# Kernel tuning notes

Measured on AMD Instinct MI355X. Metric: run time of the kernel, lower is better.

## Reference

```python
import jax, jax.numpy as jnp
import numpy as np
from jax import lax

B, C_IN, T = 256, 1, 1632
HID, CB_DIM, NUM_TOK, NUM_Q = 64, 512, 1024, 2


def conv_k2s2(x, W, b):
    # Conv1d(kernel=2, stride=2): x [B,Ci,T] -> [B,Co,T//2]; W [Co,Ci,2]
    Bx, Ci, Tx = x.shape
    xr = x.reshape(Bx, Ci, Tx // 2, 2)
    return jnp.einsum('bitk,oik->bot', xr, W) + b[None, :, None]


def convT_k2s2(x, W, b):
    # ConvTranspose1d(kernel=2, stride=2): x [B,Ci,T] -> [B,Co,2T]; W [Ci,Co,2] (torch layout)
    Bx, Ci, Tx = x.shape
    y = jnp.einsum('bit,iok->botk', x, W)  # [B,Co,T,2]
    Co = W.shape[1]
    return y.reshape(Bx, Co, 2 * Tx) + b[None, :, None]


def conv1x1(x, W, b):
    # W [Co,Ci]
    return jnp.einsum('bit,oi->bot', x, W) + b[None, :, None]


def residual_vq(x, codebooks):
    # x [B,t,D]; codebooks [NUM_Q, NUM_TOK, D]. Euclidean argmin + straight-through.
    residual = x
    quantized_out = jnp.zeros_like(x)
    all_idx, all_loss = [], []
    for q in range(codebooks.shape[0]):
        cb = codebooks[q]  # [N,D]
        # squared euclidean distance, single large GEMM
        d2 = (jnp.sum(residual ** 2, -1, keepdims=True)
              - 2.0 * jnp.einsum('btd,nd->btn', residual, cb)
              + jnp.sum(cb ** 2, -1))  # [B,t,N]
        idx = jnp.argmin(d2, axis=-1)  # [B,t]
        quant = cb[idx]  # gather [B,t,D]
        # commitment loss (codebook treated as fixed / EMA-updated)
        loss = jnp.mean((lax.stop_gradient(quant) - residual) ** 2)
        # straight-through estimator
        quant_st = residual + lax.stop_gradient(quant - residual)
        residual = residual - lax.stop_gradient(quant)
        quantized_out = quantized_out + quant_st
        all_idx.append(idx)
        all_loss.append(loss)
    return quantized_out, jnp.stack(all_idx, -1), jnp.stack(all_loss)


def setup_inputs() -> dict:
    key = jax.random.key(0)
    ks = jax.random.split(key, 16)
    s = 0.02
    return {
        'img': jax.random.normal(ks[0], (B, C_IN, T), jnp.float32),
        'W_e1': jax.random.normal(ks[1], (HID, C_IN, 2), jnp.float32) * s,
        'b_e1': jnp.zeros((HID,), jnp.float32),
        'W_e2': jax.random.normal(ks[2], (HID, HID, 2), jnp.float32) * s,
        'b_e2': jnp.zeros((HID,), jnp.float32),
        'W_e3': jax.random.normal(ks[3], (CB_DIM, HID), jnp.float32) * s,
        'b_e3': jnp.zeros((CB_DIM,), jnp.float32),
        'codebooks': jax.random.normal(ks[4], (NUM_Q, NUM_TOK, CB_DIM), jnp.float32),
        'Wt_d1': jax.random.normal(ks[5], (CB_DIM, HID, 2), jnp.float32) * s,
        'b_d1': jnp.zeros((HID,), jnp.float32),
        'Wt_d2': jax.random.normal(ks[6], (HID, HID, 2), jnp.float32) * s,
        'b_d2': jnp.zeros((HID,), jnp.float32),
        'W_d3': jax.random.normal(ks[7], (C_IN, HID), jnp.float32) * s,
        'b_d3': jnp.zeros((C_IN,), jnp.float32),
    }


def reference(img, W_e1, b_e1, W_e2, b_e2, W_e3, b_e3, codebooks,
              Wt_d1, b_d1, Wt_d2, b_d2, W_d3, b_d3):
    # encoder
    h = jax.nn.relu(conv_k2s2(img, W_e1, b_e1))
    h = jax.nn.relu(conv_k2s2(h, W_e2, b_e2))
    encoded = conv1x1(h, W_e3, b_e3)  # [B,512,408]
    # residual VQ over tokens
    x = jnp.transpose(encoded, (0, 2, 1))  # b c t -> b t c
    quantized, indices, commit_loss = residual_vq(x, codebooks)
    quantized = jnp.transpose(quantized, (0, 2, 1))  # b t c -> b c t
    # decoder
    d = jax.nn.relu(convT_k2s2(quantized, Wt_d1, b_d1))
    d = jax.nn.relu(convT_k2s2(d, Wt_d2, b_d2))
    out = conv1x1(d, W_d3, b_d3)  # [B,1,1632]
    recon_loss = jnp.mean((img - out) ** 2)
    return out, recon_loss, commit_loss, indices, quantized
```

## Files before the change

### kernel.cpp

```cpp
#include <hip/hip_runtime.h>

#define NB    256
#define TLEN  1632
#define HIDC  64
#define CBD   512
#define NTOK  1024
#define T2L   816
#define T4L   408
#define MTOK  (NB*T4L)
#define M2TOK (NB*T2L)
#define MOUT  (NB*TLEN)

#define DO_OUT    ((size_t)0)
#define DO_RECON  ((size_t)417792)
#define DO_IDX    ((size_t)417795)
#define DO_QUANT  ((size_t)626691)

typedef unsigned short u16;
typedef unsigned long long u64;
typedef __attribute__((ext_vector_type(8))) short short8;
typedef __attribute__((ext_vector_type(4))) float f32x4;
typedef __attribute__((ext_vector_type(8))) _Float16 half8;
typedef __attribute__((ext_vector_type(4))) _Float16 half4;

static constexpr size_t OFF_XR  = 0;
static constexpr size_t OFF_H1  = OFF_XR + (size_t)MTOK*512;
static constexpr size_t OFF_H2  = OFF_H1 + (size_t)NB*T2L*64;
static constexpr size_t OFF_BE2 = OFF_H2 + (size_t)NB*T4L*64;
static constexpr size_t OFF_BD1 = OFF_BE2 + 8192;
static constexpr size_t OFF_BD2 = OFF_BD1 + 65536;
static constexpr size_t OFF_BX1 = OFF_BD2 + 8192;
static constexpr size_t OFF_BX2 = OFF_BX1 + 128;
static constexpr size_t OFF_ZB  = OFF_BX2 + 128;
static constexpr size_t OFF_C2  = OFF_ZB + 128;
static constexpr size_t OFF_SLOT= OFF_C2 + 2048;
static constexpr size_t OFF_IDXI= OFF_SLOT + 1536;
static constexpr size_t OFF_KEYS= OFF_IDXI + (size_t)MTOK*2;
static constexpr size_t OFF_FC  = OFF_KEYS + (size_t)MTOK*4;
static constexpr size_t OFF_FLAG= OFF_FC + 4;
static constexpr size_t OFF_CBH = OFF_FLAG + (size_t)MTOK*2;
static constexpr size_t OFF_CBL = OFF_CBH + 524288;
static constexpr size_t OFF_P0  = OFF_CBL + 524288;
static constexpr size_t OFF_P1  = OFF_P0 + 131072;
static constexpr size_t OFF_PAIRS = OFF_P1 + 131072;

__device__ inline u64 shfl_xor_u64_w16(u64 v, int m) {
    unsigned lo = (unsigned)v, hi = (unsigned)(v >> 32);
    lo = __shfl_xor(lo, m, 16);
    hi = __shfl_xor(hi, m, 16);
    return (((u64)hi) << 32) | lo;
}
__device__ inline u64 packkey(float d, int n) {
    unsigned u = __float_as_uint(d);
    u = (u & 0x80000000u) ? ~u : (u | 0x80000000u);
    return (((u64)u) << 32) | (unsigned)n;
}
__device__ inline float unpackd(u64 k) {
    unsigned u = (unsigned)(k >> 32);
    u = (u & 0x80000000u) ? (u & 0x7fffffffu) : ~u;
    return __uint_as_float(u);
}
__device__ inline void merge2(u64& k1, u64& k2, u64 o1, u64 o2) {
    u64 n1 = (k1 < o1) ? k1 : o1;
    u64 hi = (k1 < o1) ? o1 : k1;
    u64 cand = (k1 <= o1) ? k2 : o2;
    u64 n2 = (hi < cand) ? hi : cand;
    k1 = n1; k2 = n2;
}
__device__ inline half4 cvt_h4(float4 v) {
    half4 h;
    h.x = (_Float16)v.x; h.y = (_Float16)v.y;
    h.z = (_Float16)v.z; h.w = (_Float16)v.w;
    return h;
}

__global__ void setup_kernel(const float* __restrict__ We2, const float* __restrict__ Wtd1,
                             const float* __restrict__ Wtd2, const float* __restrict__ bd1,
                             const float* __restrict__ bd2, const float* __restrict__ cbs,
                             float* __restrict__ Be2, float* __restrict__ Bd1,
                             float* __restrict__ Bd2, float* __restrict__ bx1, float* __restrict__ bx2,
                             u16* __restrict__ cbh, u16* __restrict__ cbl, float* __restrict__ c2) {
    size_t t = (size_t)blockIdx.x * 256 + threadIdx.x;
    {
        float4 v = *(const float4*)(cbs + t * 4);
        half4 h = cvt_h4(v);
        half4 l;
        l.x = (_Float16)(v.x - (float)h.x);
        l.y = (_Float16)(v.y - (float)h.y);
        l.z = (_Float16)(v.z - (float)h.z);
        l.w = (_Float16)(v.w - (float)h.w);
        *(half4*)&cbh[t * 4] = h;
        *(half4*)&cbl[t * 4] = l;
    }
    {
        int w = (int)(t >> 6);
        int lane = threadIdx.x & 63;
        if (w < 2048) {
            const float* r = cbs + (size_t)w * 512;
            float4 a = *(const float4*)(r + lane * 8);
            float4 b = *(const float4*)(r + lane * 8 + 4);
            float s = a.x*a.x + a.y*a.y + a.z*a.z + a.w*a.w + b.x*b.x + b.y*b.y + b.z*b.z + b.w*b.w;
            #pragma unroll
            for (int o = 32; o > 0; o >>= 1) s += __shfl_down(s, o, 64);
            if (lane == 0) c2[w] = s;
        }
    }
    size_t stride = (size_t)gridDim.x * 256;
    for (size_t x = t; x < 64 * 128; x += stride) {
        int c = (int)(x >> 7), k = (int)(x & 127);
        Be2[x] = We2[c * 128 + ((k & 63) << 1) + (k >> 6)];
    }
    for (size_t x = t; x < 128 * 512; x += stride) {
        int n = (int)(x >> 9), k = (int)(x & 511);
        Bd1[x] = Wtd1[k * 128 + n];
    }
    for (size_t x = t; x < 128 * 64; x += stride) {
        int n = (int)(x >> 6), k = (int)(x & 63);
        Bd2[x] = Wtd2[k * 128 + n];
    }
    for (size_t x = t; x < 128; x += stride) { bx1[x] = bd1[x >> 1]; bx2[x] = bd2[x >> 1]; }
}

__global__ void enc1_kernel(const float* __restrict__ img, const float* __restrict__ W,
                            const float* __restrict__ bias, float* __restrict__ h1) {
    int idx = blockIdx.x * 256 + threadIdx.x;
    int c = idx & 63;
    int t = (idx >> 6) % T2L;
    int b = idx / (64 * T2L);
    float v = W[c * 2] * img[(size_t)b * TLEN + 2 * t] +
              W[c * 2 + 1] * img[(size_t)b * TLEN + 2 * t + 1] + bias[c];
    h1[idx] = fmaxf(v, 0.f);
}

__global__ __launch_bounds__(256) void gemm_nt(const float* __restrict__ A, const float* __restrict__ Bw,
                        const float* __restrict__ bias, float* __restrict__ C,
                        int M, int N, int K, int amode, int relu) {
    __shared__ float As[32][132];
    __shared__ float Bs[32][68];
    int m0 = blockIdx.x * 128;
    int n0 = blockIdx.y * 64;
    int tid = threadIdx.x;
    int tx = tid & 15;
    int ty = tid >> 4;
    float acc[8][4];
    #pragma unroll
    for (int i = 0; i < 8; ++i)
        #pragma unroll
        for (int j = 0; j < 4; ++j) acc[i][j] = 0.f;

    for (int k0 = 0; k0 < K; k0 += 32) {
        #pragma unroll
        for (int i = 0; i < 4; ++i) {
            int idx = tid + i * 256;
            int row = idx >> 3;
            int kq = idx & 7;
            int m = m0 + row;
            size_t base;
            if (amode == 0) base = (size_t)m * K;
            else            base = (size_t)(((m / T4L) * T2L + 2 * (m % T4L)) * 64);
            float4 v = *(const float4*)(A + base + k0 + kq * 4);
            int kk = kq * 4;
            As[kk + 0][row] = v.x; As[kk + 1][row] = v.y;
            As[kk + 2][row] = v.z; As[kk + 3][row] = v.w;
        }
        #pragma unroll
        for (int i = 0; i < 2; ++i) {
            int idx = tid + i * 256;
            int row = idx >> 3;
            int kq = idx & 7;
            float4 v = *(const float4*)(Bw + (size_t)(n0 + row) * K + k0 + kq * 4);
            int kk = kq * 4;
            Bs[kk + 0][row] = v.x; Bs[kk + 1][row] = v.y;
            Bs[kk + 2][row] = v.z; Bs[kk + 3][row] = v.w;
        }
        __syncthreads();
        #pragma unroll
        for (int kk = 0; kk < 32; ++kk) {
            float a[8], bf[4];
            float4 a0 = *(const float4*)&As[kk][ty * 8];
            float4 a1 = *(const float4*)&As[kk][ty * 8 + 4];
            a[0]=a0.x; a[1]=a0.y; a[2]=a0.z; a[3]=a0.w;
            a[4]=a1.x; a[5]=a1.y; a[6]=a1.z; a[7]=a1.w;
            float4 b0 = *(const float4*)&Bs[kk][tx * 4];
            bf[0]=b0.x; bf[1]=b0.y; bf[2]=b0.z; bf[3]=b0.w;
            #pragma unroll
            for (int i = 0; i < 8; ++i)
                #pragma unroll
                for (int j = 0; j < 4; ++j) acc[i][j] += a[i] * bf[j];
        }
        __syncthreads();
    }
    #pragma unroll
    for (int i = 0; i < 8; ++i) {
        int m = m0 + ty * 8 + i;
        float4 v;
        v.x = acc[i][0] + bias[n0 + tx * 4 + 0];
        v.y = acc[i][1] + bias[n0 + tx * 4 + 1];
        v.z = acc[i][2] + bias[n0 + tx * 4 + 2];
        v.w = acc[i][3] + bias[n0 + tx * 4 + 3];
        if (relu) { v.x=fmaxf(v.x,0.f); v.y=fmaxf(v.y,0.f); v.z=fmaxf(v.z,0.f); v.w=fmaxf(v.w,0.f); }
        *(float4*)(C + (size_t)m * N + n0 + tx * 4) = v;
    }
}

template<int Q1>
__global__ __launch_bounds__(256, 2) void vq_f16_top2(
    const float* __restrict__ A, const u16* __restrict__ cbh, const u16* __restrict__ cbl,
    const float* __restrict__ c2, const u64* __restrict__ prevkeys, const float* __restrict__ cb0,
    u64* __restrict__ pairs)
{
    __shared__ __align__(16) u16 As[128 * 40];
    __shared__ __align__(16) u16 Bh[256 * 40];
    __shared__ __align__(16) u16 Bl[Q1 ? 256 * 40 : 8];
    constexpr int BI = Q1 ? 8 : 4;
    int tid = threadIdx.x;
    int n0 = blockIdx.x * 256, m0 = blockIdx.y * 128;
    int lane = tid & 63, wid = tid >> 6;
    int lm = lane & 15, quad = lane >> 4;
    int wm = wid >> 1, wn = wid & 1;

    f32x4 acc[4][8];
    #pragma unroll
    for (int i = 0; i < 4; ++i)
        #pragma unroll
        for (int j = 0; j < 8; ++j) acc[i][j] = (f32x4){0.f, 0.f, 0.f, 0.f};

    int ar[4], acq[4];
    size_t coff[4];
    #pragma unroll
    for (int i = 0; i < 4; ++i) {
        int idx = tid + i * 256;
        ar[i] = idx >> 3; acq[i] = idx & 7;
        if (Q1) {
            int i0 = (int)(prevkeys[m0 + ar[i]] & 0xFFFFFFFFull);
            coff[i] = (size_t)i0 * 512;
        }
    }

    for (int k0 = 0; k0 < 512; k0 += 32) {
        float4 av[4];
        #pragma unroll
        for (int i = 0; i < 4; ++i) {
            av[i] = *(const float4*)(A + (size_t)(m0 + ar[i]) * 512 + k0 + acq[i] * 4);
            if (Q1) {
                float4 cv = *(const float4*)(cb0 + coff[i] + k0 + acq[i] * 4);
                av[i].x -= cv.x; av[i].y -= cv.y; av[i].z -= cv.z; av[i].w -= cv.w;
            }
        }
        short8 bv[BI];
        int br[BI], bcc[BI], bpl[BI];
        #pragma unroll
        for (int i = 0; i < BI; ++i) {
            int idx = tid + i * 256;
            if (Q1) {
                br[i] = idx >> 3; int sub = idx & 7;
                bcc[i] = sub & 3; bpl[i] = sub >> 2;
                const u16* src = bpl[i] ? cbl : cbh;
                bv[i] = *(const short8*)(src + (size_t)(n0 + br[i]) * 512 + k0 + bcc[i] * 8);
            } else {
                br[i] = idx >> 2; bcc[i] = idx & 3; bpl[i] = 0;
                bv[i] = *(const short8*)(cbh + (size_t)(n0 + br[i]) * 512 + k0 + bcc[i] * 8);
            }
        }
        __syncthreads();
        #pragma unroll
        for (int i = 0; i < 4; ++i) {
            *(half4*)&As[ar[i] * 40 + acq[i] * 4] = cvt_h4(av[i]);
        }
        #pragma unroll
        for (int i = 0; i < BI; ++i) {
            u16* dst = (Q1 && bpl[i]) ? Bl : Bh;
            *(short8*)&dst[br[i] * 40 + bcc[i] * 8] = bv[i];
        }
        __syncthreads();
        half8 ah[4];
        #pragma unroll
        for (int mt = 0; mt < 4; ++mt) {
            int r = wm * 64 + mt * 16 + lm;
            ah[mt] = *(const half8*)&As[r * 40 + quad * 8];
        }
        #pragma unroll
        for (int nt = 0; nt < 8; ++nt) {
            int rn = wn * 128 + nt * 16 + lm;
            half8 bh = *(const half8*)&Bh[rn * 40 + quad * 8];
            if (Q1) {
                half8 bl = *(const half8*)&Bl[rn * 40 + quad * 8];
                #pragma unroll
                for (int mt = 0; mt < 4; ++mt) {
                    acc[mt][nt] = __builtin_amdgcn_mfma_f32_16x16x32_f16(ah[mt], bl, acc[mt][nt], 0, 0, 0);
                    acc[mt][nt] = __builtin_amdgcn_mfma_f32_16x16x32_f16(ah[mt], bh, acc[mt][nt], 0, 0, 0);
                }
            } else {
                #pragma unroll
                for (int mt = 0; mt < 4; ++mt) {
                    acc[mt][nt] = __builtin_amdgcn_mfma_f32_16x16x32_f16(ah[mt], bh, acc[mt][nt], 0, 0, 0);
                }
            }
        }
    }
    float c2v[8];
    #pragma unroll
    for (int nt = 0; nt < 8; ++nt) c2v[nt] = c2[n0 + wn * 128 + nt * 16 + lm];

    __syncthreads();
    u64* scr = (u64*)As;
    #pragma unroll
    for (int mt = 0; mt < 4; ++mt) {
        #pragma unroll
        for (int rg = 0; rg < 4; ++rg) {
            int tl = wm * 64 + mt * 16 + quad * 4 + rg;
            u64 k1 = ~0ull, k2 = ~0ull;
            #pragma unroll
            for (int nt = 0; nt < 8; ++nt) {
                float d = c2v[nt] - 2.0f * acc[mt][nt][rg];
                u64 k = packkey(d, n0 + wn * 128 + nt * 16 + lm);
                if (k < k1) { k2 = k1; k1 = k; } else if (k < k2) { k2 = k; }
            }
            #pragma unroll
            for (int s = 1; s < 16; s <<= 1) {
                u64 o1 = shfl_xor_u64_w16(k1, s);
                u64 o2 = shfl_xor_u64_w16(k2, s);
                merge2(k1, k2, o1, o2);
            }
            if (lm == 0) { scr[wn * 256 + tl * 2] = k1; scr[wn * 256 + tl * 2 + 1] = k2; }
        }
    }
    __syncthreads();
    if (tid < 128) {
        u64 a1 = scr[tid * 2], a2 = scr[tid * 2 + 1];
        merge2(a1, a2, scr[256 + tid * 2], scr[256 + tid * 2 + 1]);
        size_t base = (size_t)(m0 + tid) * 8 + blockIdx.x * 2;
        pairs[base] = a1; pairs[base + 1] = a2;
    }
}

__global__ void vq_reduce(const u64* __restrict__ pairs, u64* __restrict__ keybuf,
                          int* __restrict__ fc, int* __restrict__ flaglist, float tau) {
    int m = blockIdx.x * 256 + threadIdx.x;
    const u64* p = pairs + (size_t)m * 8;
    u64 k1 = ~0ull, k2 = ~0ull;
    #pragma unroll
    for (int i = 0; i < 8; ++i) {
        u64 k = p[i];
        if (k < k1) { k2 = k1; k1 = k; } else if (k < k2) { k2 = k; }
    }
    keybuf[m] = k1;
    if (unpackd(k2) - unpackd(k1) < tau) {
        int pos = atomicAdd(fc, 1);
        flaglist[pos] = m;
    }
}

__global__ void vq_rescue(const float* __restrict__ xr, const float* __restrict__ cb,
                          const float* __restrict__ c2, const float* __restrict__ cb0,
                          const u64* __restrict__ prevkeys,
                          const int* __restrict__ fc, const int* __restrict__ flaglist,
                          u64* __restrict__ keybuf) {
    __shared__ u64 red[4];
    int cnt = *fc;
    int lane = threadIdx.x & 63, wid = threadIdx.x >> 6;
    for (int f = blockIdx.x; f < cnt; f += gridDim.x) {
        int m = flaglist[f];
        float4 rv0 = *(const float4*)(xr + (size_t)m * 512 + lane * 8);
        float4 rv1 = *(const float4*)(xr + (size_t)m * 512 + lane * 8 + 4);
        if (cb0) {
            size_t co = (size_t)(prevkeys[m] & 0xFFFFFFFFull) * 512;
            float4 c0 = *(const float4*)(cb0 + co + lane * 8);
            float4 c1 = *(const float4*)(cb0 + co + lane * 8 + 4);
            rv0.x -= c0.x; rv0.y -= c0.y; rv0.z -= c0.z; rv0.w -= c0.w;
            rv1.x -= c1.x; rv1.y -= c1.y; rv1.z -= c1.z; rv1.w -= c1.w;
        }
        u64 best = ~0ull;
        for (int c = wid * 256; c < wid * 256 + 256; ++c) {
            const float* cp = cb + (size_t)c * 512 + lane * 8;
            float4 c0 = *(const float4*)cp;
            float4 c1 = *(const float4*)(cp + 4);
            float p = rv0.x*c0.x + rv0.y*c0.y + rv0.z*c0.z + rv0.w*c0.w
                    + rv1.x*c1.x + rv1.y*c1.y + rv1.z*c1.z + rv1.w*c1.w;
            #pragma unroll
            for (int s = 1; s < 64; s <<= 1) p += __shfl_xor(p, s, 64);
            u64 k = packkey(c2[c] - 2.0f * p, c);
            if (k < best) best = k;
        }
        if (lane == 0) red[wid] = best;
        __syncthreads();
        if (threadIdx.x == 0) {
            u64 b = red[0];
            if (red[1] < b) b = red[1];
            if (red[2] < b) b = red[2];
            if (red[3] < b) b = red[3];
            keybuf[m] = b;
        }
        __syncthreads();
    }
}

__global__ void commit_idx_kernel(const float* __restrict__ xr,
                                  const float* __restrict__ cb0f, const float* __restrict__ cb1f,
                                  const u64* __restrict__ keys0, const u64* __restrict__ keys1,
                                  float* __restrict__ idx_f, int* __restrict__ idx_i,
                                  float* __restrict__ slots) {
    int tid = threadIdx.x;
    int lane = tid & 63;
    int m = blockIdx.x * 4 + (tid >> 6);
    unsigned i0 = (unsigned)(keys0[m] & 0xFFFFFFFFull);
    unsigned i1 = (unsigned)(keys1[m] & 0xFFFFFFFFull);
    const float* x = xr + (size_t)m * 512 + lane * 8;
    const float* c0 = cb0f + (size_t)i0 * 512 + lane * 8;
    const float* c1 = cb1f + (size_t)i1 * 512 + lane * 8;
    float4 x0 = *(const float4*)x, x1 = *(const float4*)(x + 4);
    float4 a0 = *(const float4*)c0, a1 = *(const float4*)(c0 + 4);
    float4 b0 = *(const float4*)c1, b1 = *(const float4*)(c1 + 4);
    x0.x -= a0.x; x0.y -= a0.y; x0.z -= a0.z; x0.w -= a0.w;
    x1.x -= a1.x; x1.y -= a1.y; x1.z -= a1.z; x1.w -= a1.w;
    float s1 = x0.x*x0.x + x0.y*x0.y + x0.z*x0.z + x0.w*x0.w
             + x1.x*x1.x + x1.y*x1.y + x1.z*x1.z + x1.w*x1.w;
    x0.x -= b0.x; x0.y -= b0.y; x0.z -= b0.z; x0.w -= b0.w;
    x1.x -= b1.x; x1.y -= b1.y; x1.z -= b1.z; x1.w -= b1.w;
    float s2 = x0.x*x0.x + x0.y*x0.y + x0.z*x0.z + x0.w*x0.w
             + x1.x*x1.x + x1.y*x1.y + x1.z*x1.z + x1.w*x1.w;
    #pragma unroll
    for (int o = 32; o > 0; o >>= 1) { s1 += __shfl_down(s1, o, 64); s2 += __shfl_down(s2, o, 64); }
    if (lane == 0) {
        atomicAdd(&slots[512 + (m & 511)], s1);
        atomicAdd(&slots[1024 + (m & 511)], s2);
        idx_f[(size_t)m * 2]     = (float)i0;
        idx_f[(size_t)m * 2 + 1] = (float)i1;
        idx_i[m * 2] = (int)i0;
        idx_i[m * 2 + 1] = (int)i1;
    }
}

__global__ void quant_out_kernel(const float* __restrict__ cb0, const float* __restrict__ cb1,
                                 const int* __restrict__ idxi, float* __restrict__ out4) {
    __shared__ float buf[64][129];
    __shared__ int i0s[64], i1s[64];
    int b = blockIdx.x;
    int t0 = blockIdx.y * 64;
    int c0 = blockIdx.z * 128;
    int tid = threadIdx.x;
    if (tid < 64) {
        int t = t0 + tid;
        int i0 = 0, i1 = 0;
        if (t < T4L) { i0 = idxi[(b * T4L + t) * 2]; i1 = idxi[(b * T4L + t) * 2 + 1]; }
        i0s[tid] = i0; i1s[tid] = i1;
    }
    __syncthreads();
    int cl = tid & 127, th = tid >> 7;
    for (int t = th; t < 64; t += 2) {
        if (t0 + t < T4L)
            buf[t][cl] = cb0[(size_t)i0s[t] * 512 + c0 + cl] + cb1[(size_t)i1s[t] * 512 + c0 + cl];
    }
    __syncthreads();
    int lane = tid & 63, ch = tid >> 6;
    for (int cc = ch; cc < 128; cc += 4) {
        int t = t0 + lane;
        if (t < T4L) out4[((size_t)b * 512 + c0 + cc) * T4L + t] = buf[lane][cc];
    }
}

__global__ void d1_gather_kernel(const float* __restrict__ P0, const float* __restrict__ P1,
                                 const int* __restrict__ idxi, const float* __restrict__ bx1,
                                 float* __restrict__ d1) {
    int x = blockIdx.x * 256 + threadIdx.x;
    int n = x & 127;
    int m = x >> 7;
    int b = m / T4L, t = m % T4L;
    int i0 = idxi[m * 2], i1 = idxi[m * 2 + 1];
    float v = P0[i0 * 128 + n] + P1[i1 * 128 + n] + bx1[n];
    v = fmaxf(v, 0.f);
    d1[((size_t)(b * T2L + 2 * t + (n & 1))) * 64 + (n >> 1)] = v;
}

__global__ __launch_bounds__(256) void dec2_fused(
    const float* __restrict__ d1, const float* __restrict__ Bd2, const float* __restrict__ bx2,
    const float* __restrict__ W3, const float* __restrict__ b3, const float* __restrict__ img,
    float* __restrict__ out, float* __restrict__ slots)
{
    __shared__ float As[32][132];
    __shared__ float Bs[32][132];
    __shared__ float w3s[64];
    int m0 = blockIdx.x * 128;
    int tid = threadIdx.x;
    int tx = tid & 15;
    int ty = tid >> 4;
    if (tid < 64) w3s[tid] = W3[tid];
    float acc[8][8];
    #pragma unroll
    for (int i = 0; i < 8; ++i)
        #pragma unroll
        for (int j = 0; j < 8; ++j) acc[i][j] = 0.f;

    for (int k0 = 0; k0 < 64; k0 += 32) {
        #pragma unroll
        for (int i = 0; i < 4; ++i) {
            int idx = tid + i * 256;
            int row = idx >> 3;
            int kq = idx & 7;
            float4 v = *(const float4*)(d1 + (size_t)(m0 + row) * 64 + k0 + kq * 4);
            int kk = kq * 4;
            As[kk + 0][row] = v.x; As[kk + 1][row] = v.y;
            As[kk + 2][row] = v.z; As[kk + 3][row] = v.w;
        }
        #pragma unroll
        for (int i = 0; i < 4; ++i) {
            int idx = tid + i * 256;
            int row = idx >> 3;
            int kq = idx & 7;
            float4 v = *(const float4*)(Bd2 + (size_t)row * 64 + k0 + kq * 4);
            int kk = kq * 4;
            Bs[kk + 0][row] = v.x; Bs[kk + 1][row] = v.y;
            Bs[kk + 2][row] = v.z; Bs[kk + 3][row] = v.w;
        }
        __syncthreads();
        #pragma unroll
        for (int kk = 0; kk < 32; ++kk) {
            float a[8], bf[8];
            float4 a0 = *(const float4*)&As[kk][ty * 8];
            float4 a1 = *(const float4*)&As[kk][ty * 8 + 4];
            a[0]=a0.x; a[1]=a0.y; a[2]=a0.z; a[3]=a0.w;
            a[4]=a1.x; a[5]=a1.y; a[6]=a1.z; a[7]=a1.w;
            float4 b0 = *(const float4*)&Bs[kk][tx * 4];
            float4 b1 = *(const float4*)&Bs[kk][64 + tx * 4];
            bf[0]=b0.x; bf[1]=b0.y; bf[2]=b0.z; bf[3]=b0.w;
            bf[4]=b1.x; bf[5]=b1.y; bf[6]=b1.z; bf[7]=b1.w;
            #pragma unroll
            for (int i = 0; i < 8; ++i)
                #pragma unroll
                for (int j = 0; j < 8; ++j) acc[i][j] += a[i] * bf[j];
        }
        __syncthreads();
    }
    float bb3 = b3[0];
    float local = 0.f;
    #pragma unroll
    for (int i = 0; i < 8; ++i) {
        float s0 = 0.f, s1 = 0.f;
        #pragma unroll
        for (int j = 0; j < 4; ++j) {
            int n = tx * 4 + j;
            float v = fmaxf(acc[i][j] + bx2[n], 0.f);
            float w = w3s[n >> 1];
            if (j & 1) s1 += w * v; else s0 += w * v;
            int n2 = 64 + tx * 4 + j;
            float v2 = fmaxf(acc[i][j + 4] + bx2[n2], 0.f);
            float w2 = w3s[n2 >> 1];
            if (j & 1) s1 += w2 * v2; else s0 += w2 * v2;
        }
        #pragma unroll
        for (int o = 8; o > 0; o >>= 1) { s0 += __shfl_down(s0, o, 16); s1 += __shfl_down(s1, o, 16); }
        if (tx == 0) {
            int m = m0 + ty * 8 + i;
            int b = m / T2L, t2 = m % T2L;
            size_t o0 = (size_t)b * TLEN + 2 * t2;
            float v0 = s0 + bb3, v1 = s1 + bb3;
            out[o0] = v0; out[o0 + 1] = v1;
            float e0 = img[o0] - v0, e1 = img[o0 + 1] - v1;
            local += e0 * e0 + e1 * e1;
        }
    }
    if (tx == 0) atomicAdd(&slots[(blockIdx.x * 16 + ty) & 511], local);
}

__global__ void finalize_kernel(const float* __restrict__ slots, float* __restrict__ out_scalars) {
    __shared__ float red[256];
    int tid = threadIdx.x;
    for (int which = 0; which < 3; ++which) {
        float s = slots[which * 512 + tid] + slots[which * 512 + tid + 256];
        red[tid] = s; __syncthreads();
        for (int st = 128; st > 0; st >>= 1) { if (tid < st) red[tid] += red[tid + st]; __syncthreads(); }
        if (tid == 0) {
            float denom = (which == 0) ? (float)MOUT : (float)((size_t)MTOK * 512);
            out_scalars[which] = red[0] / denom;
        }
        __syncthreads();
    }
}

extern "C" void kernel_launch(void* const* d_in, const int* in_sizes, int n_in,
                              void* d_out, int out_size, void* d_ws, size_t ws_size,
                              hipStream_t stream) {
    const float* img  = (const float*)d_in[0];
    const float* We1  = (const float*)d_in[1];
    const float* be1  = (const float*)d_in[2];
    const float* We2  = (const float*)d_in[3];
    const float* be2  = (const float*)d_in[4];
    const float* We3  = (const float*)d_in[5];
    const float* be3  = (const float*)d_in[6];
    const float* cbs  = (const float*)d_in[7];
    const float* Wtd1 = (const float*)d_in[8];
    const float* bd1  = (const float*)d_in[9];
    const float* Wtd2 = (const float*)d_in[10];
    const float* bd2  = (const float*)d_in[11];
    const float* Wd3  = (const float*)d_in[12];
    const float* bd3  = (const float*)d_in[13];

    float* w = (float*)d_ws;
    float* xr   = w + OFF_XR;
    float* h1   = w + OFF_H1;
    float* h2   = w + OFF_H2;
    float* Be2  = w + OFF_BE2;
    float* Bd1  = w + OFF_BD1;
    float* Bd2  = w + OFF_BD2;
    float* bx1  = w + OFF_BX1;
    float* bx2  = w + OFF_BX2;
    float* zerob= w + OFF_ZB;
    float* c2   = w + OFF_C2;
    float* slots= w + OFF_SLOT;
    int*   idxi = (int*)(w + OFF_IDXI);
    u64*   keys = (u64*)(w + OFF_KEYS);
    int*   fc   = (int*)(w + OFF_FC);
    int*   flag = (int*)(w + OFF_FLAG);
    u16*   cbh  = (u16*)(w + OFF_CBH);
    u16*   cbl  = (u16*)(w + OFF_CBL);
    float* P0   = w + OFF_P0;
    float* P1   = w + OFF_P1;
    u64*   pairs= (u64*)(w + OFF_PAIRS);

    float* outp = (float*)d_out;
    float* out0   = outp + DO_OUT;
    float* oscal  = outp + DO_RECON;
    float* idxf   = outp + DO_IDX;
    float* qout   = outp + DO_QUANT;

    hipMemsetAsync(slots, 0, 1536 * sizeof(float), stream);
    hipMemsetAsync(fc, 0, 2 * sizeof(int), stream);
    hipMemsetAsync(zerob, 0, 128 * sizeof(float), stream);

    setup_kernel<<<1024, 256, 0, stream>>>(We2, Wtd1, Wtd2, bd1, bd2, cbs,
                                           Be2, Bd1, Bd2, bx1, bx2, cbh, cbl, c2);

    const float* cb1p = cbs + (size_t)NTOK * CBD;

    gemm_nt<<<dim3(8, 2), 256, 0, stream>>>(cbs,  Bd1, zerob, P0, 1024, 128, 512, 0, 0);
    gemm_nt<<<dim3(8, 2), 256, 0, stream>>>(cb1p, Bd1, zerob, P1, 1024, 128, 512, 0, 0);

    enc1_kernel<<<(NB * T2L * HIDC) / 256, 256, 0, stream>>>(img, We1, be1, h1);
    gemm_nt<<<dim3(MTOK / 128, 1), 256, 0, stream>>>(h1, Be2, be2, h2, MTOK, 64, 128, 1, 1);
    gemm_nt<<<dim3(MTOK / 128, 8), 256, 0, stream>>>(h2, We3, be3, xr, MTOK, 512, 64, 0, 0);

    vq_f16_top2<0><<<dim3(4, MTOK / 128), 256, 0, stream>>>(xr, cbh, cbl, c2, nullptr, nullptr, pairs);
    vq_reduce<<<MTOK / 256, 256, 0, stream>>>(pairs, keys, fc + 0, flag, 0.05f);
    vq_rescue<<<1024, 256, 0, stream>>>(xr, cbs, c2, nullptr, nullptr, fc + 0, flag, keys);
    vq_f16_top2<1><<<dim3(4, MTOK / 128), 256, 0, stream>>>(xr, cbh + (size_t)NTOK * 512, cbl + (size_t)NTOK * 512,
                                                            c2 + NTOK, keys, cbs, pairs);
    vq_reduce<<<MTOK / 256, 256, 0, stream>>>(pairs, keys + MTOK, fc + 1, flag + MTOK, 0.08f);
    vq_rescue<<<1024, 256, 0, stream>>>(xr, cb1p, c2 + NTOK, cbs, keys, fc + 1, flag + MTOK, keys + MTOK);

    commit_idx_kernel<<<MTOK / 4, 256, 0, stream>>>(xr, cbs, cb1p, keys, keys + MTOK, idxf, idxi, slots);

    quant_out_kernel<<<dim3(NB, 7, 4), 256, 0, stream>>>(cbs, cb1p, idxi, qout);

    d1_gather_kernel<<<(MTOK * 128) / 256, 256, 0, stream>>>(P0, P1, idxi, bx1, h1);
    dec2_fused<<<M2TOK / 128, 256, 0, stream>>>(h1, Bd2, bx2, Wd3, bd3, img, out0, slots);

    finalize_kernel<<<1, 256, 0, stream>>>(slots, oscal);
}
```

Before: 1.233 ms.

## Load VQ MFMA operands directly from global memory, bypassing LDS staging

Replaces the LDS-tiled VQ distance GEMM with a version where each wave loads its A and codebook fragments straight from global memory into registers, and fully unrolls the k-loop. This removes shared-memory stores and the two barriers per k-step. In exchange, data shared across waves is re-read from global memory, accesses are narrower per row, and register pressure rises.

```diff
diff --git a/kernel.cpp b/kernel.cpp
--- a/kernel.cpp
+++ b/kernel.cpp
@@ -73,6 +73,14 @@
     h.z = (_Float16)v.z; h.w = (_Float16)v.w;
     return h;
 }
+__device__ inline half8 cvt_h8(float4 v0, float4 v1) {
+    half8 h;
+    h[0] = (_Float16)v0.x; h[1] = (_Float16)v0.y;
+    h[2] = (_Float16)v0.z; h[3] = (_Float16)v0.w;
+    h[4] = (_Float16)v1.x; h[5] = (_Float16)v1.y;
+    h[6] = (_Float16)v1.z; h[7] = (_Float16)v1.w;
+    return h;
+}
 
 __global__ void setup_kernel(const float* __restrict__ We2, const float* __restrict__ Wtd1,
                              const float* __restrict__ Wtd2, const float* __restrict__ bd1,
@@ -204,15 +212,12 @@
 }
 
 template<int Q1>
-__global__ __launch_bounds__(256, 2) void vq_f16_top2(
+__global__ __launch_bounds__(256, 2) void vq_f16_reg(
     const float* __restrict__ A, const u16* __restrict__ cbh, const u16* __restrict__ cbl,
     const float* __restrict__ c2, const u64* __restrict__ prevkeys, const float* __restrict__ cb0,
     u64* __restrict__ pairs)
 {
-    __shared__ __align__(16) u16 As[128 * 40];
-    __shared__ __align__(16) u16 Bh[256 * 40];
-    __shared__ __align__(16) u16 Bl[Q1 ? 256 * 40 : 8];
-    constexpr int BI = Q1 ? 8 : 4;
+    __shared__ u64 scr[512];
     int tid = threadIdx.x;
     int n0 = blockIdx.x * 256, m0 = blockIdx.y * 128;
     int lane = tid & 63, wid = tid >> 6;
@@ -225,66 +230,43 @@
         #pragma unroll
         for (int j = 0; j < 8; ++j) acc[i][j] = (f32x4){0.f, 0.f, 0.f, 0.f};
 
-    int ar[4], acq[4];
-    size_t coff[4];
-    #pragma unroll
-    for (int i = 0; i < 4; ++i) {
-        int idx = tid + i * 256;
-        ar[i] = idx >> 3; acq[i] = idx & 7;
+    int aoff[4], coff[4], boff[8];
+    #pragma unroll
+    for (int mt = 0; mt < 4; ++mt) {
+        int r = m0 + wm * 64 + mt * 16 + lm;
+        aoff[mt] = r * 512;
         if (Q1) {
-            int i0 = (int)(prevkeys[m0 + ar[i]] & 0xFFFFFFFFull);
-            coff[i] = (size_t)i0 * 512;
-        }
-    }
-
+            int i0 = (int)(prevkeys[r] & 0xFFFFFFFFull);
+            coff[mt] = i0 * 512;
+        }
+    }
+    #pragma unroll
+    for (int nt = 0; nt < 8; ++nt) {
+        int rn = n0 + wn * 128 + nt * 16 + lm;
+        boff[nt] = rn * 512;
+    }
+
+    #pragma unroll
     for (int k0 = 0; k0 < 512; k0 += 32) {
-        float4 av[4];
-        #pragma unroll
-        for (int i = 0; i < 4; ++i) {
-            av[i] = *(const float4*)(A + (size_t)(m0 + ar[i]) * 512 + k0 + acq[i] * 4);
+        int kc = k0 + quad * 8;
+        half8 ah[4];
+        #pragma unroll
+        for (int mt = 0; mt < 4; ++mt) {
+            float4 v0 = *(const float4*)(A + aoff[mt] + kc);
+            float4 v1 = *(const float4*)(A + aoff[mt] + kc + 4);
             if (Q1) {
-                float4 cv = *(const float4*)(cb0 + coff[i] + k0 + acq[i] * 4);
-                av[i].x -= cv.x; av[i].y -= cv.y; av[i].z -= cv.z; av[i].w -= cv.w;
+                float4 c0 = *(const float4*)(cb0 + coff[mt] + kc);
+                float4 c1 = *(const float4*)(cb0 + coff[mt] + kc + 4);
+                v0.x -= c0.x; v0.y -= c0.y; v0.z -= c0.z; v0.w -= c0.w;
+                v1.x -= c1.x; v1.y -= c1.y; v1.z -= c1.z; v1.w -= c1.w;
             }
-        }
-        short8 bv[BI];
-        int br[BI], bcc[BI], bpl[BI];
-        #pragma unroll
-        for (int i = 0; i < BI; ++i) {
-            int idx = tid + i * 256;
+            ah[mt] = cvt_h8(v0, v1);
+        }
+        #pragma unroll
+        for (int nt = 0; nt < 8; ++nt) {
+            half8 bh = *(const half8*)(cbh + boff[nt] + kc);
             if (Q1) {
-                br[i] = idx >> 3; int sub = idx & 7;
-                bcc[i] = sub & 3; bpl[i] = sub >> 2;
-                const u16* src = bpl[i] ? cbl : cbh;
-                bv[i] = *(const short8*)(src + (size_t)(n0 + br[i]) * 512 + k0 + bcc[i] * 8);
-            } else {
-                br[i] = idx >> 2; bcc[i] = idx & 3; bpl[i] = 0;
-                bv[i] = *(const short8*)(cbh + (size_t)(n0 + br[i]) * 512 + k0 + bcc[i] * 8);
-            }
-        }
-        __syncthreads();
-        #pragma unroll
-        for (int i = 0; i < 4; ++i) {
-            *(half4*)&As[ar[i] * 40 + acq[i] * 4] = cvt_h4(av[i]);
-        }
-        #pragma unroll
-        for (int i = 0; i < BI; ++i) {
-            u16* dst = (Q1 && bpl[i]) ? Bl : Bh;
-            *(short8*)&dst[br[i] * 40 + bcc[i] * 8] = bv[i];
-        }
-        __syncthreads();
-        half8 ah[4];
-        #pragma unroll
-        for (int mt = 0; mt < 4; ++mt) {
-            int r = wm * 64 + mt * 16 + lm;
-            ah[mt] = *(const half8*)&As[r * 40 + quad * 8];
-        }
-        #pragma unroll
-        for (int nt = 0; nt < 8; ++nt) {
-            int rn = wn * 128 + nt * 16 + lm;
-            half8 bh = *(const half8*)&Bh[rn * 40 + quad * 8];
-            if (Q1) {
-                half8 bl = *(const half8*)&Bl[rn * 40 + quad * 8];
+                half8 bl = *(const half8*)(cbl + boff[nt] + kc);
                 #pragma unroll
                 for (int mt = 0; mt < 4; ++mt) {
                     acc[mt][nt] = __builtin_amdgcn_mfma_f32_16x16x32_f16(ah[mt], bl, acc[mt][nt], 0, 0, 0);
@@ -298,12 +280,11 @@
             }
         }
     }
+
     float c2v[8];
     #pragma unroll
     for (int nt = 0; nt < 8; ++nt) c2v[nt] = c2[n0 + wn * 128 + nt * 16 + lm];
 
-    __syncthreads();
-    u64* scr = (u64*)As;
     #pragma unroll
     for (int mt = 0; mt < 4; ++mt) {
         #pragma unroll
@@ -639,11 +620,11 @@
     gemm_nt<<<dim3(MTOK / 128, 1), 256, 0, stream>>>(h1, Be2, be2, h2, MTOK, 64, 128, 1, 1);
     gemm_nt<<<dim3(MTOK / 128, 8), 256, 0, stream>>>(h2, We3, be3, xr, MTOK, 512, 64, 0, 0);
 
-    vq_f16_top2<0><<<dim3(4, MTOK / 128), 256, 0, stream>>>(xr, cbh, cbl, c2, nullptr, nullptr, pairs);
+    vq_f16_reg<0><<<dim3(4, MTOK / 128), 256, 0, stream>>>(xr, cbh, nullptr, c2, nullptr, nullptr, pairs);
     vq_reduce<<<MTOK / 256, 256, 0, stream>>>(pairs, keys, fc + 0, flag, 0.05f);
     vq_rescue<<<1024, 256, 0, stream>>>(xr, cbs, c2, nullptr, nullptr, fc + 0, flag, keys);
-    vq_f16_top2<1><<<dim3(4, MTOK / 128), 256, 0, stream>>>(xr, cbh + (size_t)NTOK * 512, cbl + (size_t)NTOK * 512,
-                                                            c2 + NTOK, keys, cbs, pairs);
+    vq_f16_reg<1><<<dim3(4, MTOK / 128), 256, 0, stream>>>(xr, cbh + (size_t)NTOK * 512, cbl + (size_t)NTOK * 512,
+                                                           c2 + NTOK, keys, cbs, pairs);
     vq_reduce<<<MTOK / 256, 256, 0, stream>>>(pairs, keys + MTOK, fc + 1, flag + MTOK, 0.08f);
     vq_rescue<<<1024, 256, 0, stream>>>(xr, cb1p, c2 + NTOK, cbs, keys, fc + 1, flag + MTOK, keys + MTOK);
 
```

Measured after the change: 1.818 ms. 1.48x slower.
